# Performance work log

Measured on AMD Instinct MI355X. Metric: run time of the kernel, lower is better.

The kernel has to match this reference:

```python
import jax, jax.numpy as jnp
import numpy as np

B, N = 2, 8192
FUN, EMB = 7, 3
H = 512
HEADS = 8
DH = H // HEADS  # 64
G = 32           # slice_num
L = 4            # n_layers
OUT = 4
MLP_H = 4 * H


def _ln(x, g, b, eps=1e-5):
    m = x.mean(-1, keepdims=True)
    v = ((x - m) ** 2).mean(-1, keepdims=True)
    return (x - m) * jax.lax.rsqrt(v + eps) * g + b


def _forward(fun, emb, W_pre1, b_pre1, W_pre2, b_pre2, placeholder,
             ln1_g, ln1_b, Wfx, bfx, Wx, bx, Wslice, bslice, temp,
             Wq, Wk, Wv, Wo, bo, ln2_g, ln2_b, Wm1, bm1, Wm2, bm2,
             lnf_g, lnf_b, Wout, bout):
    b, n = fun.shape[0], fun.shape[1]
    gelu = lambda z: jax.nn.gelu(z, approximate=False)  # torch nn.GELU default (erf)
    # preprocess MLP (n_layers=0, res=False): act(pre(x)) -> post
    x = jnp.concatenate([emb, fun], axis=-1)            # [B,N,EMB+FUN]
    fx = gelu(x @ W_pre1 + b_pre1) @ W_pre2 + b_pre2    # [B,N,H]
    fx = fx + placeholder
    scale = DH ** -0.5
    for l in range(L):
        # --- physics attention (irregular mesh) ---
        h = _ln(fx, ln1_g[l], ln1_b[l])
        fx_mid = (h @ Wfx[l] + bfx[l]).reshape(b, n, HEADS, DH)  # bnhd
        x_mid = (h @ Wx[l] + bx[l]).reshape(b, n, HEADS, DH)
        logits = jnp.einsum('bnhd,dg->bnhg', x_mid, Wslice[l]) + bslice[l]
        sw = jax.nn.softmax(logits / temp[l][None, None, :, None], axis=-1)  # bnhg
        slice_mass = sw.sum(axis=1)                                   # bhg
        token = jnp.einsum('bnhd,bnhg->bhgd', fx_mid, sw)
        token = token / (slice_mass[..., None] + 1e-5)                # bhgd
        q = token @ Wq[l]
        k = token @ Wk[l]
        v = token @ Wv[l]
        attn = jax.nn.softmax(jnp.einsum('bhgd,bhkd->bhgk', q, k) * scale, axis=-1)
        out_tok = jnp.einsum('bhgk,bhkd->bhgd', attn, v)
        out = jnp.einsum('bhgd,bnhg->bnhd', out_tok, sw).reshape(b, n, H)
        fx = out @ Wo[l] + bo[l] + fx
        # --- LN + MLP (hidden = 4H) with residual ---
        h2 = _ln(fx, ln2_g[l], ln2_b[l])
        fx = gelu(h2 @ Wm1[l] + bm1[l]) @ Wm2[l] + bm2[l] + fx
    # last-layer head: LN -> Linear(out_dim)
    return _ln(fx, lnf_g, lnf_b) @ Wout + bout


def setup_inputs() -> dict:
    key = jax.random.key(0)
    ks = iter(jax.random.split(key, 64))
    nrm = lambda shape, s=0.02: jax.random.normal(next(ks), shape, jnp.float32) * s
    return dict(
        fun=jax.random.normal(next(ks), (B, N, FUN), jnp.float32),
        emb=jax.random.normal(next(ks), (B, N, EMB), jnp.float32),
        W_pre1=nrm((FUN + EMB, 2 * H)), b_pre1=jnp.zeros((2 * H,), jnp.float32),
        W_pre2=nrm((2 * H, H)), b_pre2=jnp.zeros((H,), jnp.float32),
        placeholder=nrm((H,), 1.0),
        ln1_g=jnp.ones((L, H), jnp.float32), ln1_b=jnp.zeros((L, H), jnp.float32),
        Wfx=nrm((L, H, H)), bfx=jnp.zeros((L, H), jnp.float32),
        Wx=nrm((L, H, H)), bx=jnp.zeros((L, H), jnp.float32),
        Wslice=nrm((L, DH, G), 0.1), bslice=jnp.zeros((L, G), jnp.float32),
        temp=jnp.full((L, HEADS), 0.5, jnp.float32),
        Wq=nrm((L, DH, DH)), Wk=nrm((L, DH, DH)), Wv=nrm((L, DH, DH)),
        Wo=nrm((L, H, H)), bo=jnp.zeros((L, H), jnp.float32),
        ln2_g=jnp.ones((L, H), jnp.float32), ln2_b=jnp.zeros((L, H), jnp.float32),
        Wm1=nrm((L, H, MLP_H)), bm1=jnp.zeros((L, MLP_H), jnp.float32),
        Wm2=nrm((L, MLP_H, H)), bm2=jnp.zeros((L, H), jnp.float32),
        lnf_g=jnp.ones((H,), jnp.float32), lnf_b=jnp.zeros((H,), jnp.float32),
        Wout=nrm((H, OUT)), bout=jnp.zeros((OUT,), jnp.float32),
    )


def reference(fun, emb, W_pre1, b_pre1, W_pre2, b_pre2, placeholder,
              ln1_g, ln1_b, Wfx, bfx, Wx, bx, Wslice, bslice, temp,
              Wq, Wk, Wv, Wo, bo, ln2_g, ln2_b, Wm1, bm1, Wm2, bm2,
              lnf_g, lnf_b, Wout, bout):
    return _forward(fun, emb, W_pre1, b_pre1, W_pre2, b_pre2, placeholder,
                    ln1_g, ln1_b, Wfx, bfx, Wx, bx, Wslice, bslice, temp,
                    Wq, Wk, Wv, Wo, bo, ln2_g, ln2_b, Wm1, bm1, Wm2, bm2,
                    lnf_g, lnf_b, Wout, bout)
```

## Files before the change

### kernel.cpp

```cpp
#include <hip/hip_runtime.h>
#include <hip/hip_bf16.h>
#include <cstdint>
#include <cstddef>

typedef float  f32x4  __attribute__((ext_vector_type(4)));
typedef __bf16 bf16x8 __attribute__((ext_vector_type(8)));
typedef __bf16 bf16x4 __attribute__((ext_vector_type(4)));

#define DEV __device__ __forceinline__

DEV float gelu_f(float x){ return 0.5f * x * (1.0f + erff(x * 0.70710678118654752f)); }

#define WAIT_LGKM0 0xC07F

static constexpr size_t OFF_FX     = 0;
static constexpr size_t OFF_H      = 33554432;
static constexpr size_t OFF_REGA   = 50331648;
static constexpr size_t OFF_FXMID  = OFF_REGA;
static constexpr size_t OFF_SW     = OFF_REGA + 16777216;
static constexpr size_t OFF_MLPH   = OFF_REGA;
static constexpr size_t OFF_H1     = OFF_REGA;
static constexpr size_t OFF_OUTB   = OFF_REGA + 67108864;
static constexpr size_t OFF_PT     = OFF_OUTB + 16777216;
static constexpr size_t OFF_PTM    = OFF_PT + 2097152;
static constexpr size_t OFF_OT     = OFF_PTM + 32768;
static constexpr size_t OFF_WT     = OFF_OT + 131072;
static constexpr size_t OFF_BIAS   = OFF_WT + 23068672;

__global__ __launch_bounds__(256) void wtrans_k(const float* __restrict__ W, __bf16* __restrict__ Wt,
                                                int K, int N, size_t wstride, size_t wtstride)
{
  __shared__ float tile[64][65];
  W  += (size_t)blockIdx.z * wstride;
  Wt += (size_t)blockIdx.z * wtstride;
  int t = threadIdx.x;
  int k0 = blockIdx.x * 64, n0 = blockIdx.y * 64;
  #pragma unroll
  for (int i = 0; i < 16; i++){
    int e = t + 256*i; int kk = e >> 6, nn = e & 63;
    tile[kk][nn] = W[(size_t)(k0+kk)*N + n0+nn];
  }
  __syncthreads();
  #pragma unroll
  for (int i = 0; i < 16; i++){
    int e = t + 256*i; int nn = e >> 6, kk = e & 63;
    Wt[(size_t)(n0+nn)*K + k0+kk] = (__bf16)tile[kk][nn];
  }
}

__global__ __launch_bounds__(128) void prep_wxs_k(const float* __restrict__ Wx, const float* __restrict__ Wsl,
                                                  const float* __restrict__ bx, const float* __restrict__ bsl,
                                                  const float* __restrict__ temp,
                                                  __bf16* __restrict__ Btcat, float* __restrict__ bcat)
{
  __shared__ float wsc[64];
  int l = blockIdx.y;
  const float* Wx_l  = Wx  + (size_t)l*262144;
  const float* Wsl_l = Wsl + l*2048;
  const float* bx_l  = bx  + l*512;
  const float* bsl_l = bsl + l*32;
  __bf16* Wt_l = Btcat + (size_t)l*393216 + (size_t)512*512;
  float* blog_l = bcat + l*768 + 512;
  int hg = blockIdx.x; int h = hg >> 5, g = hg & 31;
  int t = threadIdx.x;
  if (t < 64) wsc[t] = Wsl_l[t*32 + g];
  __syncthreads();
  float invt = 1.0f / temp[l*8 + h];
  #pragma unroll
  for (int cc = 0; cc < 4; cc++){
    int c = t + cc*128;
    float a = 0.f;
    for (int d = 0; d < 64; d++) a += Wx_l[(size_t)c*512 + h*64 + d] * wsc[d];
    Wt_l[(size_t)hg*512 + c] = (__bf16)(a * invt);
  }
  if (t == 0){
    float a = 0.f;
    for (int d = 0; d < 64; d++) a += bx_l[h*64 + d] * wsc[d];
    blog_l[hg] = (a + bsl_l[g]) * invt;
  }
}

__global__ __launch_bounds__(256) void bias_setup_k(const float* __restrict__ b_pre2, const float* __restrict__ placeholder,
                                                    const float* __restrict__ bfx,
                                                    float* __restrict__ bpre2p, float* __restrict__ bcat)
{
  int i = blockIdx.x*256 + threadIdx.x;
  if (i < 512) bpre2p[i] = b_pre2[i] + placeholder[i];
  else if (i < 2560){
    int j = i - 512; int l = j >> 9, c = j & 511;
    bcat[l*768 + c] = bfx[l*512 + c];
  }
}

__global__ __launch_bounds__(256) void preproc1_k(const float* __restrict__ fun, const float* __restrict__ emb,
                                                  const float* __restrict__ W1, const float* __restrict__ b1,
                                                  __bf16* __restrict__ h1)
{
  __shared__ float w1l[10][1024];
  int t = threadIdx.x;
  for (int i = t*4; i < 10240; i += 1024) *(f32x4*)&w1l[0][i] = *(const f32x4*)&W1[i];
  __syncthreads();
  f32x4 bv = *(const f32x4*)&b1[t*4];
  int r0 = blockIdx.x * 4;
  for (int r = 0; r < 4; r++){
    int m = r0 + r;
    const float* er = emb + (size_t)m*3;
    const float* fr = fun + (size_t)m*7;
    float x[10];
    x[0]=er[0]; x[1]=er[1]; x[2]=er[2];
    #pragma unroll
    for (int c = 0; c < 7; c++) x[3+c] = fr[c];
    f32x4 acc = bv;
    #pragma unroll
    for (int c = 0; c < 10; c++){
      f32x4 wv = *(const f32x4*)&w1l[c][t*4];
      acc += x[c] * wv;
    }
    __bf16* op = h1 + (size_t)m*1024 + t*4;
    #pragma unroll
    for (int e = 0; e < 4; e++) op[e] = (__bf16)gelu_f(acc[e]);
  }
}

template<int EPI, int BN>
__global__ __launch_bounds__(512) void gemm_wide(const __bf16* __restrict__ A, const __bf16* __restrict__ Bt,
                                                 const float* __restrict__ bias, const float* __restrict__ res,
                                                 void* __restrict__ outp, void* __restrict__ outp2,
                                                 int N, int lgK)
{
  constexpr int NSUB_B = BN/16;
  constexpr int S = 16 + NSUB_B;
  constexpr int Q = S/8;
  constexpr int NJ = BN/32;
  __shared__ bf16x8 ldsAB[2][S][64];
  const int tid = threadIdx.x;
  const int w = tid >> 6, lane = tid & 63;
  const int lm = lane & 15, lq = lane >> 4;
  const int wr = w >> 1, wc = w & 1;
  const int m0 = blockIdx.x * 256, n0 = blockIdx.y * BN;
  const int niter = 1 << (lgK - 5);

  const __bf16* gp[Q];
  #pragma unroll
  for (int q = 0; q < Q; q++){
    int f = w*Q + q;
    gp[q] = (f < 16)
      ? A  + (((size_t)(m0 + f*16 + lm)) << lgK) + lq*8
      : Bt + (((size_t)(n0 + (f-16)*16 + lm)) << lgK) + lq*8;
  }

  bf16x8 r[Q];
  #pragma unroll
  for (int q = 0; q < Q; q++){ r[q] = *(const bf16x8*)gp[q]; gp[q] += 32; }

  f32x4 acc[4][NJ] = {};

  for (int i = 0; i < niter; ++i){
    __builtin_amdgcn_s_barrier();
    const unsigned buf = (unsigned)i & 1u;
    #pragma unroll
    for (int q = 0; q < Q; q++)
      ldsAB[buf][w*Q + q][lane] = r[q];
    if (i + 1 < niter){
      #pragma unroll
      for (int q = 0; q < Q; q++){ r[q] = *(const bf16x8*)gp[q]; gp[q] += 32; }
    }
    __builtin_amdgcn_s_waitcnt(WAIT_LGKM0);
    __builtin_amdgcn_s_barrier();
    bf16x8 af[4], bfr[NJ];
    #pragma unroll
    for (int ii = 0; ii < 4; ii++)  af[ii]  = ldsAB[buf][wr*4 + ii][lane];
    #pragma unroll
    for (int jj = 0; jj < NJ; jj++) bfr[jj] = ldsAB[buf][16 + wc*NJ + jj][lane];
    #pragma unroll
    for (int ii = 0; ii < 4; ii++)
      #pragma unroll
      for (int jj = 0; jj < NJ; jj++)
        acc[ii][jj] = __builtin_amdgcn_mfma_f32_16x16x32_bf16(af[ii], bfr[jj], acc[ii][jj], 0, 0, 0);
  }

  if (EPI == 4 && blockIdx.y == 2){
    float* swp = (float*)outp2;
    #pragma unroll
    for (int ii = 0; ii < 4; ii++){
      int row0 = m0 + wr*64 + ii*16 + lq*4;
      #pragma unroll
      for (int hp = 0; hp < 4; hp++){
        int j0 = hp*2, j1 = j0 + 1;
        int h = wc*4 + hp;
        float b0 = bias[512 + wc*128 + j0*16 + lm];
        float b1 = bias[512 + wc*128 + j1*16 + lm];
        #pragma unroll
        for (int r2 = 0; r2 < 4; r2++){
          int row = row0 + r2;
          float v0 = acc[ii][j0][r2] + b0;
          float v1 = acc[ii][j1][r2] + b1;
          float mx = fmaxf(v0, v1);
          #pragma unroll
          for (int msk = 8; msk; msk >>= 1) mx = fmaxf(mx, __shfl_xor(mx, msk));
          float e0 = expf(v0 - mx), e1 = expf(v1 - mx);
          float ss = e0 + e1;
          #pragma unroll
          for (int msk = 8; msk; msk >>= 1) ss += __shfl_xor(ss, msk);
          float inv = 1.f / ss;
          int b = row >> 13, n = row & 8191;
          float* op = swp + ((size_t)(b*8 + h)*8192 + n)*32;
          op[lm]      = e0 * inv;
          op[16 + lm] = e1 * inv;
        }
      }
    }
    return;
  }

  #pragma unroll
  for (int ii = 0; ii < 4; ii++){
    int row0 = m0 + wr*64 + ii*16 + lq*4;
    #pragma unroll
    for (int jj = 0; jj < NJ; jj++){
      int col = n0 + wc*(BN/2) + jj*16 + lm;
      float bv = bias[col];
      #pragma unroll
      for (int r2 = 0; r2 < 4; r2++){
        size_t idx = (size_t)(row0 + r2)*N + col;
        float v = acc[ii][jj][r2] + bv;
        if (EPI == 2) v += res[idx];
        if (EPI == 1)      ((__bf16*)outp)[idx] = (__bf16)gelu_f(v);
        else if (EPI == 4) ((__bf16*)outp)[idx] = (__bf16)v;
        else               ((float*)outp)[idx]  = v;
      }
    }
  }
}

__global__ __launch_bounds__(256) void ln_k(const float* __restrict__ x, const float* __restrict__ g,
                                            const float* __restrict__ b, __bf16* __restrict__ out)
{
  int w = threadIdx.x >> 6, lane = threadIdx.x & 63;
  int row = blockIdx.x*4 + w;
  const float* xr = x + (size_t)row*512 + lane*8;
  float v[8];
  *(f32x4*)&v[0] = *(const f32x4*)xr;
  *(f32x4*)&v[4] = *(const f32x4*)(xr + 4);
  float s = 0.f, sq = 0.f;
  #pragma unroll
  for (int e = 0; e < 8; e++){ s += v[e]; sq += v[e]*v[e]; }
  #pragma unroll
  for (int off = 32; off; off >>= 1){ s += __shfl_xor(s, off); sq += __shfl_xor(sq, off); }
  float mean = s * (1.f/512.f);
  float var  = sq * (1.f/512.f) - mean*mean;
  float rstd = rsqrtf(var + 1e-5f);
  float gv[8], bv[8];
  *(f32x4*)&gv[0] = *(const f32x4*)(g + lane*8);
  *(f32x4*)&gv[4] = *(const f32x4*)(g + lane*8 + 4);
  *(f32x4*)&bv[0] = *(const f32x4*)(b + lane*8);
  *(f32x4*)&bv[4] = *(const f32x4*)(b + lane*8 + 4);
  __bf16* op = out + (size_t)row*512 + lane*8;
  #pragma unroll
  for (int e = 0; e < 8; e++) op[e] = (__bf16)((v[e]-mean)*rstd*gv[e] + bv[e]);
}

__global__ __launch_bounds__(256) void token_part_k(const __bf16* __restrict__ fxmid, const float* __restrict__ sw,
                                                    float* __restrict__ pt, float* __restrict__ ptm)
{
  __shared__ float fxl[32][64];
  __shared__ float swl[32][32];
  int t = threadIdx.x;
  int chunk = blockIdx.x, bh = blockIdx.y;
  int b = bh >> 3, h = bh & 7;
  int d = t & 63, gg = (t >> 6) * 8;
  float acc[8] = {0,0,0,0,0,0,0,0};
  float macc = 0.f;
  for (int s = 0; s < 16; s++){
    int nbase = chunk*512 + s*32;
    __syncthreads();
    #pragma unroll
    for (int i = 0; i < 2; i++){
      int e = t + 256*i; int rv = e >> 4, c4 = e & 15;
      bf16x4 v = *(const bf16x4*)&fxmid[((size_t)(b*8192 + nbase + rv))*512 + h*64 + c4*4];
      fxl[rv][c4*4+0] = (float)v[0];
      fxl[rv][c4*4+1] = (float)v[1];
      fxl[rv][c4*4+2] = (float)v[2];
      fxl[rv][c4*4+3] = (float)v[3];
    }
    { int rv = t >> 3, c4 = t & 7;
      *(f32x4*)&swl[rv][c4*4] = *(const f32x4*)&sw[((size_t)bh*8192 + nbase + rv)*32 + c4*4]; }
    __syncthreads();
    for (int nn = 0; nn < 32; nn++){
      float f = fxl[nn][d];
      #pragma unroll
      for (int jj = 0; jj < 8; jj++) acc[jj] += f * swl[nn][gg+jj];
    }
    if (t < 32){ for (int nn = 0; nn < 32; nn++) macc += swl[nn][t]; }
  }
  int cb = chunk*16 + bh;
  #pragma unroll
  for (int jj = 0; jj < 8; jj++)
    pt[((size_t)cb*32 + gg + jj)*64 + d] = acc[jj];
  if (t < 32) ptm[cb*32 + t] = macc;
}

__global__ __launch_bounds__(256) void attn_k(const float* __restrict__ pt, const float* __restrict__ ptm,
                                              const float* __restrict__ Wq, const float* __restrict__ Wk,
                                              const float* __restrict__ Wv, float* __restrict__ ot)
{
  __shared__ float tok[32][64];
  __shared__ float ml[32];
  __shared__ float qq[32][65], kk2[32][65], vv[32][65];
  __shared__ float at[32][33];
  int t = threadIdx.x, bh = blockIdx.x;
  if (t < 32){
    float s = 0.f;
    for (int c = 0; c < 16; c++) s += ptm[(c*16 + bh)*32 + t];
    ml[t] = s + 1e-5f;
  }
  __syncthreads();
  #pragma unroll
  for (int i = 0; i < 8; i++){
    int e = t + 256*i; int g = e >> 6, d = e & 63;
    float s = 0.f;
    for (int c = 0; c < 16; c++) s += pt[((size_t)(c*16 + bh)*32 + g)*64 + d];
    tok[g][d] = s / ml[g];
  }
  __syncthreads();
  #pragma unroll
  for (int i = 0; i < 8; i++){
    int e = t + 256*i; int g = e >> 6, j = e & 63;
    float aq = 0.f, ak = 0.f, av = 0.f;
    for (int d = 0; d < 64; d++){
      float tv = tok[g][d];
      aq += tv * Wq[d*64 + j];
      ak += tv * Wk[d*64 + j];
      av += tv * Wv[d*64 + j];
    }
    qq[g][j] = aq; kk2[g][j] = ak; vv[g][j] = av;
  }
  __syncthreads();
  #pragma unroll
  for (int i = 0; i < 4; i++){
    int e = t + 256*i; int g = e >> 5, j2 = e & 31;
    float s2 = 0.f;
    for (int d = 0; d < 64; d++) s2 += qq[g][d] * kk2[j2][d];
    at[g][j2] = s2 * 0.125f;
  }
  __syncthreads();
  if (t < 32){
    float mx = at[t][0];
    for (int j = 1; j < 32; j++) mx = fmaxf(mx, at[t][j]);
    float ss = 0.f;
    for (int j = 0; j < 32; j++){ float e2 = expf(at[t][j]-mx); at[t][j] = e2; ss += e2; }
    float inv = 1.f / ss;
    for (int j = 0; j < 32; j++) at[t][j] *= inv;
  }
  __syncthreads();
  #pragma unroll
  for (int i = 0; i < 8; i++){
    int e = t + 256*i; int g = e >> 6, d = e & 63;
    float s3 = 0.f;
    for (int j = 0; j < 32; j++) s3 += at[g][j] * vv[j][d];
    ot[(size_t)bh*2048 + e] = s3;
  }
}

__global__ __launch_bounds__(256) void deslice_k(const float* __restrict__ ot, const float* __restrict__ sw,
                                                 __bf16* __restrict__ outb)
{
  __shared__ float otl[32][64];
  __shared__ float swl[128][36];
  int t = threadIdx.x;
  int chunk = blockIdx.x, bh = blockIdx.y;
  int b = bh >> 3, h = bh & 7;
  int n0 = chunk*128;
  #pragma unroll
  for (int i = 0; i < 8; i++){
    int e = t + 256*i;
    otl[e>>6][e&63] = ot[(size_t)bh*2048 + e];
  }
  {
    int r = t >> 1, half = t & 1;
    const float* sp = sw + ((size_t)bh*8192 + n0 + r)*32 + half*16;
    float* dp = &swl[r][half*16];
    #pragma unroll
    for (int q = 0; q < 4; q++) *(f32x4*)(dp + q*4) = *(const f32x4*)(sp + q*4);
  }
  __syncthreads();
  const int nl = t >> 4;
  const int d0 = (t & 15) * 4;
  float o[8][4] = {};
  for (int g = 0; g < 32; g++){
    f32x4 ov = *(const f32x4*)&otl[g][d0];
    #pragma unroll
    for (int p = 0; p < 8; p++){
      float s = swl[p*16 + nl][g];
      o[p][0] += s * ov[0]; o[p][1] += s * ov[1];
      o[p][2] += s * ov[2]; o[p][3] += s * ov[3];
    }
  }
  #pragma unroll
  for (int p = 0; p < 8; p++){
    int n = n0 + p*16 + nl;
    bf16x4 v;
    v[0] = (__bf16)o[p][0]; v[1] = (__bf16)o[p][1];
    v[2] = (__bf16)o[p][2]; v[3] = (__bf16)o[p][3];
    *(bf16x4*)&outb[((size_t)(b*8192 + n))*512 + h*64 + d0] = v;
  }
}

__global__ __launch_bounds__(256) void head_k(const float* __restrict__ x, const float* __restrict__ g,
                                              const float* __restrict__ b, const float* __restrict__ Wout,
                                              const float* __restrict__ bout, float* __restrict__ out)
{
  int w = threadIdx.x >> 6, lane = threadIdx.x & 63;
  int row = blockIdx.x*4 + w;
  const float* xr = x + (size_t)row*512 + lane*8;
  float v[8];
  *(f32x4*)&v[0] = *(const f32x4*)xr;
  *(f32x4*)&v[4] = *(const f32x4*)(xr + 4);
  float s = 0.f, sq = 0.f;
  #pragma unroll
  for (int e = 0; e < 8; e++){ s += v[e]; sq += v[e]*v[e]; }
  #pragma unroll
  for (int off = 32; off; off >>= 1){ s += __shfl_xor(s, off); sq += __shfl_xor(sq, off); }
  float mean = s * (1.f/512.f);
  float rstd = rsqrtf(sq * (1.f/512.f) - mean*mean + 1e-5f);
  float o[4] = {0,0,0,0};
  #pragma unroll
  for (int e = 0; e < 8; e++){
    int c = lane*8 + e;
    float yn = (v[e]-mean)*rstd*g[c] + b[c];
    const float* wr = Wout + (size_t)c*4;
    o[0] += yn*wr[0]; o[1] += yn*wr[1]; o[2] += yn*wr[2]; o[3] += yn*wr[3];
  }
  #pragma unroll
  for (int off = 32; off; off >>= 1){
    #pragma unroll
    for (int j = 0; j < 4; j++) o[j] += __shfl_xor(o[j], off);
  }
  if (lane == 0){
    #pragma unroll
    for (int j = 0; j < 4; j++) out[(size_t)row*4 + j] = o[j] + bout[j];
  }
}

extern "C" void kernel_launch(void* const* d_in, const int* in_sizes, int n_in,
                              void* d_out, int out_size, void* d_ws, size_t ws_size,
                              hipStream_t stream)
{
  const float* fun    = (const float*)d_in[0];
  const float* emb    = (const float*)d_in[1];
  const float* W_pre1 = (const float*)d_in[2];
  const float* b_pre1 = (const float*)d_in[3];
  const float* W_pre2 = (const float*)d_in[4];
  const float* b_pre2 = (const float*)d_in[5];
  const float* placeholder = (const float*)d_in[6];
  const float* ln1_g  = (const float*)d_in[7];
  const float* ln1_b  = (const float*)d_in[8];
  const float* Wfx    = (const float*)d_in[9];
  const float* bfx    = (const float*)d_in[10];
  const float* Wx     = (const float*)d_in[11];
  const float* bx     = (const float*)d_in[12];
  const float* Wslice = (const float*)d_in[13];
  const float* bslice = (const float*)d_in[14];
  const float* temp   = (const float*)d_in[15];
  const float* Wq     = (const float*)d_in[16];
  const float* Wk     = (const float*)d_in[17];
  const float* Wv     = (const float*)d_in[18];
  const float* Wo     = (const float*)d_in[19];
  const float* bo     = (const float*)d_in[20];
  const float* ln2_g  = (const float*)d_in[21];
  const float* ln2_b  = (const float*)d_in[22];
  const float* Wm1    = (const float*)d_in[23];
  const float* bm1    = (const float*)d_in[24];
  const float* Wm2    = (const float*)d_in[25];
  const float* bm2    = (const float*)d_in[26];
  const float* lnf_g  = (const float*)d_in[27];
  const float* lnf_b  = (const float*)d_in[28];
  const float* Wout   = (const float*)d_in[29];
  const float* bout   = (const float*)d_in[30];

  char* ws = (char*)d_ws;
  float*  fx     = (float*)(ws + OFF_FX);
  __bf16* hbf    = (__bf16*)(ws + OFF_H);
  __bf16* fxmid  = (__bf16*)(ws + OFF_FXMID);
  float*  sw     = (float*)(ws + OFF_SW);
  __bf16* mlph   = (__bf16*)(ws + OFF_MLPH);
  __bf16* h1bf   = (__bf16*)(ws + OFF_H1);
  __bf16* outb   = (__bf16*)(ws + OFF_OUTB);
  float*  pt     = (float*)(ws + OFF_PT);
  float*  ptm    = (float*)(ws + OFF_PTM);
  float*  ot     = (float*)(ws + OFF_OT);
  __bf16* Wpre2t = (__bf16*)(ws + OFF_WT);
  __bf16* Btcat  = (__bf16*)(ws + OFF_WT + 1048576);
  __bf16* Wot    = (__bf16*)(ws + OFF_WT + 4194304);
  __bf16* Wm1t   = (__bf16*)(ws + OFF_WT + 6291456);
  __bf16* Wm2t   = (__bf16*)(ws + OFF_WT + 14680064);
  float*  bcat   = (float*)(ws + OFF_BIAS);
  float*  bpre2p = (float*)(ws + OFF_BIAS + 4*768*4);

  wtrans_k<<<dim3(16,8,1), 256,0,stream>>>(W_pre2, Wpre2t, 1024, 512, 0, 0);
  wtrans_k<<<dim3(8,8,4),  256,0,stream>>>(Wfx, Btcat, 512, 512, 262144, 393216);
  wtrans_k<<<dim3(8,8,4),  256,0,stream>>>(Wo,  Wot,  512, 512, 262144, 262144);
  wtrans_k<<<dim3(8,32,4), 256,0,stream>>>(Wm1, Wm1t, 512, 2048, 1048576, 1048576);
  wtrans_k<<<dim3(32,8,4), 256,0,stream>>>(Wm2, Wm2t, 2048, 512, 1048576, 1048576);
  prep_wxs_k<<<dim3(256,4),128,0,stream>>>(Wx, Wslice, bx, bslice, temp, Btcat, bcat);
  bias_setup_k<<<10,256,0,stream>>>(b_pre2, placeholder, bfx, bpre2p, bcat);

  preproc1_k<<<4096,256,0,stream>>>(fun, emb, W_pre1, b_pre1, h1bf);
  gemm_wide<0,128><<<dim3(64,4),512,0,stream>>>(h1bf, Wpre2t, bpre2p, nullptr, (void*)fx, nullptr, 512, 10);

  for (int l = 0; l < 4; l++){
    ln_k<<<4096,256,0,stream>>>(fx, ln1_g + l*512, ln1_b + l*512, hbf);
    gemm_wide<4,256><<<dim3(64,3),512,0,stream>>>(hbf, Btcat + (size_t)l*393216, bcat + l*768, nullptr, (void*)fxmid, (void*)sw, 512, 9);
    token_part_k<<<dim3(16,16),256,0,stream>>>(fxmid, sw, pt, ptm);
    attn_k<<<16,256,0,stream>>>(pt, ptm, Wq + l*4096, Wk + l*4096, Wv + l*4096, ot);
    deslice_k<<<dim3(64,16),256,0,stream>>>(ot, sw, outb);
    gemm_wide<2,128><<<dim3(64,4),512,0,stream>>>(outb, Wot + (size_t)l*262144, bo + l*512, fx, (void*)fx, nullptr, 512, 9);
    ln_k<<<4096,256,0,stream>>>(fx, ln2_g + l*512, ln2_b + l*512, hbf);
    gemm_wide<1,256><<<dim3(64,8),512,0,stream>>>(hbf, Wm1t + (size_t)l*1048576, bm1 + l*2048, nullptr, (void*)mlph, nullptr, 2048, 9);
    gemm_wide<2,128><<<dim3(64,4),512,0,stream>>>(mlph, Wm2t + (size_t)l*1048576, bm2 + l*512, fx, (void*)fx, nullptr, 512, 11);
  }

  head_k<<<4096,256,0,stream>>>(fx, lnf_g, lnf_b, Wout, bout, (float*)d_out);
}
```

Baseline: 1.334 ms.

## Store GEMM operands in pre-tiled MFMA fragment layout for contiguous loads

Adds a fragment-major tiled layout (fm_off) for bf16 GEMM operands: activations written by LN, preproc, deslice and the MLP-up epilogue, plus transposed weights, are stored in the order each 32-wide K chunk is consumed. The GEMM loader then reads each wave's 16x32 sub-tile as one fully contiguous 1KB chunk instead of strided rows. This is meant to improve global load coalescing and cut address arithmetic in the GEMM main loop. In exchange, producers now do scattered tile-indexed writes, and the MLP-up epilogue writes single bf16 elements to non-contiguous addresses.

```diff
diff --git a/kernel.cpp b/kernel.cpp
--- a/kernel.cpp
+++ b/kernel.cpp
@@ -12,6 +12,12 @@
 DEV float gelu_f(float x){ return 0.5f * x * (1.0f + erff(x * 0.70710678118654752f)); }
 
 #define WAIT_LGKM0 0xC07F
+
+DEV size_t fm_off(int m, int k, int lgT, int lgK){
+  size_t tileblk = ((size_t)(((m >> lgT) << (lgK - 5)) | (k >> 5))) << (lgT + 5);
+  int sub = (m >> 4) & ((1 << (lgT - 4)) - 1);
+  return tileblk + ((size_t)sub << 9) + (size_t)(((((k >> 3) & 3) << 4) | (m & 15)) << 3) + (k & 7);
+}
 
 static constexpr size_t OFF_FX     = 0;
 static constexpr size_t OFF_H      = 33554432;
@@ -28,7 +34,8 @@
 static constexpr size_t OFF_BIAS   = OFF_WT + 23068672;
 
 __global__ __launch_bounds__(256) void wtrans_k(const float* __restrict__ W, __bf16* __restrict__ Wt,
-                                                int K, int N, size_t wstride, size_t wtstride)
+                                                int K, int N, size_t wstride, size_t wtstride,
+                                                int lgT, int lgK)
 {
   __shared__ float tile[64][65];
   W  += (size_t)blockIdx.z * wstride;
@@ -42,9 +49,13 @@
   }
   __syncthreads();
   #pragma unroll
-  for (int i = 0; i < 16; i++){
-    int e = t + 256*i; int nn = e >> 6, kk = e & 63;
-    Wt[(size_t)(n0+nn)*K + k0+kk] = (__bf16)tile[kk][nn];
+  for (int i2 = 0; i2 < 2; i2++){
+    int c = t + 256*i2;
+    int nn = c >> 3, ck = (c & 7) * 8;
+    bf16x8 v;
+    #pragma unroll
+    for (int j = 0; j < 8; j++) v[j] = (__bf16)tile[ck+j][nn];
+    *(bf16x8*)&Wt[fm_off(n0+nn, k0+ck, lgT, lgK)] = v;
   }
 }
 
@@ -54,12 +65,13 @@
                                                   __bf16* __restrict__ Btcat, float* __restrict__ bcat)
 {
   __shared__ float wsc[64];
+  __shared__ float wrow[512];
   int l = blockIdx.y;
   const float* Wx_l  = Wx  + (size_t)l*262144;
   const float* Wsl_l = Wsl + l*2048;
   const float* bx_l  = bx  + l*512;
   const float* bsl_l = bsl + l*32;
-  __bf16* Wt_l = Btcat + (size_t)l*393216 + (size_t)512*512;
+  __bf16* Bt_l = Btcat + (size_t)l*393216;
   float* blog_l = bcat + l*768 + 512;
   int hg = blockIdx.x; int h = hg >> 5, g = hg & 31;
   int t = threadIdx.x;
@@ -71,12 +83,20 @@
     int c = t + cc*128;
     float a = 0.f;
     for (int d = 0; d < 64; d++) a += Wx_l[(size_t)c*512 + h*64 + d] * wsc[d];
-    Wt_l[(size_t)hg*512 + c] = (__bf16)(a * invt);
+    wrow[c] = a * invt;
   }
   if (t == 0){
     float a = 0.f;
     for (int d = 0; d < 64; d++) a += bx_l[h*64 + d] * wsc[d];
     blog_l[hg] = (a + bsl_l[g]) * invt;
+  }
+  __syncthreads();
+  if (t < 64){
+    int k0 = t*8;
+    bf16x8 v;
+    #pragma unroll
+    for (int j = 0; j < 8; j++) v[j] = (__bf16)wrow[k0+j];
+    *(bf16x8*)&Bt_l[fm_off(512 + hg, k0, 8, 9)] = v;
   }
 }
 
@@ -100,25 +120,32 @@
   int t = threadIdx.x;
   for (int i = t*4; i < 10240; i += 1024) *(f32x4*)&w1l[0][i] = *(const f32x4*)&W1[i];
   __syncthreads();
-  f32x4 bv = *(const f32x4*)&b1[t*4];
+  int rsel = t >> 7, c = t & 127, k0 = c*8;
+  f32x4 bv0 = *(const f32x4*)&b1[k0];
+  f32x4 bv1 = *(const f32x4*)&b1[k0+4];
   int r0 = blockIdx.x * 4;
-  for (int r = 0; r < 4; r++){
-    int m = r0 + r;
+  #pragma unroll
+  for (int p = 0; p < 2; p++){
+    int m = r0 + p*2 + rsel;
     const float* er = emb + (size_t)m*3;
     const float* fr = fun + (size_t)m*7;
     float x[10];
     x[0]=er[0]; x[1]=er[1]; x[2]=er[2];
     #pragma unroll
-    for (int c = 0; c < 7; c++) x[3+c] = fr[c];
-    f32x4 acc = bv;
-    #pragma unroll
-    for (int c = 0; c < 10; c++){
-      f32x4 wv = *(const f32x4*)&w1l[c][t*4];
-      acc += x[c] * wv;
-    }
-    __bf16* op = h1 + (size_t)m*1024 + t*4;
-    #pragma unroll
-    for (int e = 0; e < 4; e++) op[e] = (__bf16)gelu_f(acc[e]);
+    for (int cc = 0; cc < 7; cc++) x[3+cc] = fr[cc];
+    float a8[8];
+    #pragma unroll
+    for (int j = 0; j < 8; j++) a8[j] = (j < 4) ? bv0[j] : bv1[j-4];
+    #pragma unroll
+    for (int cc = 0; cc < 10; cc++){
+      float xv = x[cc];
+      #pragma unroll
+      for (int j = 0; j < 8; j++) a8[j] += xv * w1l[cc][k0+j];
+    }
+    bf16x8 v;
+    #pragma unroll
+    for (int j = 0; j < 8; j++) v[j] = (__bf16)gelu_f(a8[j]);
+    *(bf16x8*)&h1[fm_off(m, k0, 8, 10)] = v;
   }
 }
 
@@ -132,6 +159,7 @@
   constexpr int S = 16 + NSUB_B;
   constexpr int Q = S/8;
   constexpr int NJ = BN/32;
+  constexpr int BADV = BN*32;
   __shared__ bf16x8 ldsAB[2][S][64];
   const int tid = threadIdx.x;
   const int w = tid >> 6, lane = tid & 63;
@@ -141,17 +169,22 @@
   const int niter = 1 << (lgK - 5);
 
   const __bf16* gp[Q];
+  int adv[Q];
   #pragma unroll
   for (int q = 0; q < Q; q++){
     int f = w*Q + q;
-    gp[q] = (f < 16)
-      ? A  + (((size_t)(m0 + f*16 + lm)) << lgK) + lq*8
-      : Bt + (((size_t)(n0 + (f-16)*16 + lm)) << lgK) + lq*8;
+    if (f < 16){
+      gp[q] = A + (((size_t)blockIdx.x << (lgK - 5)) * 8192) + f*512 + lane*8;
+      adv[q] = 8192;
+    } else {
+      gp[q] = Bt + (((size_t)blockIdx.y << (lgK - 5)) * BADV) + (f-16)*512 + lane*8;
+      adv[q] = BADV;
+    }
   }
 
   bf16x8 r[Q];
   #pragma unroll
-  for (int q = 0; q < Q; q++){ r[q] = *(const bf16x8*)gp[q]; gp[q] += 32; }
+  for (int q = 0; q < Q; q++){ r[q] = *(const bf16x8*)gp[q]; gp[q] += adv[q]; }
 
   f32x4 acc[4][NJ] = {};
 
@@ -163,7 +196,7 @@
       ldsAB[buf][w*Q + q][lane] = r[q];
     if (i + 1 < niter){
       #pragma unroll
-      for (int q = 0; q < Q; q++){ r[q] = *(const bf16x8*)gp[q]; gp[q] += 32; }
+      for (int q = 0; q < Q; q++){ r[q] = *(const bf16x8*)gp[q]; gp[q] += adv[q]; }
     }
     __builtin_amdgcn_s_waitcnt(WAIT_LGKM0);
     __builtin_amdgcn_s_barrier();
@@ -222,12 +255,16 @@
       float bv = bias[col];
       #pragma unroll
       for (int r2 = 0; r2 < 4; r2++){
-        size_t idx = (size_t)(row0 + r2)*N + col;
+        int row = row0 + r2;
         float v = acc[ii][jj][r2] + bv;
-        if (EPI == 2) v += res[idx];
-        if (EPI == 1)      ((__bf16*)outp)[idx] = (__bf16)gelu_f(v);
-        else if (EPI == 4) ((__bf16*)outp)[idx] = (__bf16)v;
-        else               ((float*)outp)[idx]  = v;
+        if (EPI == 1){
+          ((__bf16*)outp)[fm_off(row, col, 8, 11)] = (__bf16)gelu_f(v);
+        } else {
+          size_t idx = (size_t)row*N + col;
+          if (EPI == 2) v += res[idx];
+          if (EPI == 4) ((__bf16*)outp)[idx] = (__bf16)v;
+          else          ((float*)outp)[idx]  = v;
+        }
       }
     }
   }
@@ -255,9 +292,10 @@
   *(f32x4*)&gv[4] = *(const f32x4*)(g + lane*8 + 4);
   *(f32x4*)&bv[0] = *(const f32x4*)(b + lane*8);
   *(f32x4*)&bv[4] = *(const f32x4*)(b + lane*8 + 4);
-  __bf16* op = out + (size_t)row*512 + lane*8;
-  #pragma unroll
-  for (int e = 0; e < 8; e++) op[e] = (__bf16)((v[e]-mean)*rstd*gv[e] + bv[e]);
+  bf16x8 o8;
+  #pragma unroll
+  for (int e = 0; e < 8; e++) o8[e] = (__bf16)((v[e]-mean)*rstd*gv[e] + bv[e]);
+  *(bf16x8*)&out[fm_off(row, lane*8, 8, 9)] = o8;
 }
 
 __global__ __launch_bounds__(256) void token_part_k(const __bf16* __restrict__ fxmid, const float* __restrict__ sw,
@@ -384,25 +422,28 @@
     for (int q = 0; q < 4; q++) *(f32x4*)(dp + q*4) = *(const f32x4*)(sp + q*4);
   }
   __syncthreads();
-  const int nl = t >> 4;
-  const int d0 = (t & 15) * 4;
-  float o[8][4] = {};
+  const int slot = t >> 3;
+  const int d0 = (t & 7) * 8;
+  float o[4][8] = {};
   for (int g = 0; g < 32; g++){
-    f32x4 ov = *(const f32x4*)&otl[g][d0];
-    #pragma unroll
-    for (int p = 0; p < 8; p++){
-      float s = swl[p*16 + nl][g];
-      o[p][0] += s * ov[0]; o[p][1] += s * ov[1];
-      o[p][2] += s * ov[2]; o[p][3] += s * ov[3];
-    }
-  }
-  #pragma unroll
-  for (int p = 0; p < 8; p++){
-    int n = n0 + p*16 + nl;
-    bf16x4 v;
-    v[0] = (__bf16)o[p][0]; v[1] = (__bf16)o[p][1];
-    v[2] = (__bf16)o[p][2]; v[3] = (__bf16)o[p][3];
-    *(bf16x4*)&outb[((size_t)(b*8192 + n))*512 + h*64 + d0] = v;
+    f32x4 ov0 = *(const f32x4*)&otl[g][d0];
+    f32x4 ov1 = *(const f32x4*)&otl[g][d0+4];
+    #pragma unroll
+    for (int p = 0; p < 4; p++){
+      float s = swl[p*32 + slot][g];
+      o[p][0] += s*ov0[0]; o[p][1] += s*ov0[1]; o[p][2] += s*ov0[2]; o[p][3] += s*ov0[3];
+      o[p][4] += s*ov1[0]; o[p][5] += s*ov1[1]; o[p][6] += s*ov1[2]; o[p][7] += s*ov1[3];
+    }
+  }
+  #pragma unroll
+  for (int p = 0; p < 4; p++){
+    int n = n0 + p*32 + slot;
+    int m = b*8192 + n;
+    int k = h*64 + d0;
+    bf16x8 v;
+    #pragma unroll
+    for (int j = 0; j < 8; j++) v[j] = (__bf16)o[p][j];
+    *(bf16x8*)&outb[fm_off(m, k, 8, 9)] = v;
   }
 }
 
@@ -497,11 +538,11 @@
   float*  bcat   = (float*)(ws + OFF_BIAS);
   float*  bpre2p = (float*)(ws + OFF_BIAS + 4*768*4);
 
-  wtrans_k<<<dim3(16,8,1), 256,0,stream>>>(W_pre2, Wpre2t, 1024, 512, 0, 0);
-  wtrans_k<<<dim3(8,8,4),  256,0,stream>>>(Wfx, Btcat, 512, 512, 262144, 393216);
-  wtrans_k<<<dim3(8,8,4),  256,0,stream>>>(Wo,  Wot,  512, 512, 262144, 262144);
-  wtrans_k<<<dim3(8,32,4), 256,0,stream>>>(Wm1, Wm1t, 512, 2048, 1048576, 1048576);
-  wtrans_k<<<dim3(32,8,4), 256,0,stream>>>(Wm2, Wm2t, 2048, 512, 1048576, 1048576);
+  wtrans_k<<<dim3(16,8,1), 256,0,stream>>>(W_pre2, Wpre2t, 1024, 512, 0, 0, 7, 10);
+  wtrans_k<<<dim3(8,8,4),  256,0,stream>>>(Wfx, Btcat, 512, 512, 262144, 393216, 8, 9);
+  wtrans_k<<<dim3(8,8,4),  256,0,stream>>>(Wo,  Wot,  512, 512, 262144, 262144, 7, 9);
+  wtrans_k<<<dim3(8,32,4), 256,0,stream>>>(Wm1, Wm1t, 512, 2048, 1048576, 1048576, 8, 9);
+  wtrans_k<<<dim3(32,8,4), 256,0,stream>>>(Wm2, Wm2t, 2048, 512, 1048576, 1048576, 7, 11);
   prep_wxs_k<<<dim3(256,4),128,0,stream>>>(Wx, Wslice, bx, bslice, temp, Btcat, bcat);
   bias_setup_k<<<10,256,0,stream>>>(b_pre2, placeholder, bfx, bpre2p, bcat);
 
```

Result: faster. 1.282 ms (-3.9%).
